# Kernel tuning notes

Hardware: AMD Instinct MI355X
Metric: run time of the kernel (lower is better)

## Reference

```python
import jax, jax.numpy as jnp
import numpy as np

B, H, W = 16, 32, 32
N = H * W
C_SEARCH, C_XCORR = 256, 64
C = C_SEARCH + C_XCORR          # phi_in_channels = gcn_in_channels
PHI_H = 64
GC_HID, GC_OUT = 128, 1
K_PTS = 48                       # keypoints per image
BN_EPS = 1e-5


def _build_coords_pair():
    # 8-neighbourhood pairs (distance^2 in {1,2}), exactly gen_8neigh_coords_pair
    idx = np.arange(N).reshape(H, W)
    ys, xs = np.meshgrid(np.arange(H), np.arange(W), indexing='ij')
    pairs8 = []
    for dy in (-1, 0, 1):
        for dx in (-1, 0, 1):
            if dy == 0 and dx == 0:
                continue
            ny, nx = ys + dy, xs + dx
            m = (ny >= 0) & (ny < H) & (nx >= 0) & (nx < W)
            pairs8.append(np.stack([idx[ys[m], xs[m]], idx[ny[m], nx[m]]], axis=1))
    pairs8 = np.concatenate(pairs8, 0)  # [7812, 2]
    # keypoint permutation pairs; keypoints on even coords -> disjoint from 8-neigh
    even = np.arange(0, H, 2)
    grid_idx = (even[:, None] * W + even[None, :]).reshape(-1)
    rng = np.random.default_rng(0)
    out = []
    for _ in range(B):
        kp = rng.choice(grid_idx, size=K_PTS, replace=False)
        a, b = np.meshgrid(kp, kp, indexing='ij')
        m = a != b
        kpairs = np.stack([a[m], b[m]], axis=1)  # K*(K-1) ordered pairs
        out.append(np.concatenate([kpairs, pairs8], 0))
    return np.stack(out, 0).astype(np.int32)  # [B, E, 2]


def setup_inputs() -> dict:
    key = jax.random.key(0)
    ks = jax.random.split(key, 10)
    u = lambda k, shape, s: jax.random.uniform(k, shape, jnp.float32, -s, s)
    inp = {
        'search_feature': jax.random.normal(ks[0], (B, C_SEARCH, H, W), jnp.float32),
        'xcorr_map': jax.random.normal(ks[1], (B, C_XCORR, H, W), jnp.float32),
        'coords_pair': jnp.asarray(_build_coords_pair()),
        # phi: Linear(C, PHI_H) + BN + ReLU, then Linear(PHI_H, 1) + Sigmoid
        'phi_w1': u(ks[2], (C, PHI_H), 1.0 / np.sqrt(C)),
        'phi_b1': u(ks[3], (PHI_H,), 1.0 / np.sqrt(C)),
        'bn_gamma': jnp.ones((PHI_H,), jnp.float32),
        'bn_beta': jnp.zeros((PHI_H,), jnp.float32),
        'phi_w2': u(ks[4], (PHI_H, 1), 1.0 / np.sqrt(PHI_H)),
        'phi_b2': u(ks[5], (1,), 1.0 / np.sqrt(PHI_H)),
        # GCN weights, torch init: uniform(-1/sqrt(out), 1/sqrt(out))
        'gc1_w': u(ks[6], (C, GC_HID), 1.0 / np.sqrt(GC_HID)),
        'gc2_w': u(ks[7], (GC_HID, GC_OUT), 1.0 / np.sqrt(GC_OUT)),
    }
    return inp


def reference(search_feature, xcorr_map, coords_pair, phi_w1, phi_b1,
              bn_gamma, bn_beta, phi_w2, phi_b2, gc1_w, gc2_w):
    # catted feature flattened: [B, C, N] (row-major h*W+w, matches torch view)
    feat = jnp.concatenate([search_feature, xcorr_map], axis=1).reshape(B, C, N)

    def per_image(f, pairs):  # f: [C, N], pairs: [E, 2]
        diff = jnp.abs(f[:, pairs[:, 0]] - f[:, pairs[:, 1]]).T  # [E, C]
        h = diff @ phi_w1 + phi_b1                                # [E, PHI_H]
        mu = jnp.mean(h, axis=0)
        var = jnp.var(h, axis=0)  # biased, as torch BN training mode
        h = (h - mu) / jnp.sqrt(var + BN_EPS) * bn_gamma + bn_beta
        h = jax.nn.relu(h)
        edge = jax.nn.sigmoid(h @ phi_w2 + phi_b2)[:, 0]          # [E]
        adj = jnp.zeros((N, N), jnp.float32).at[pairs[:, 0], pairs[:, 1]].set(edge)
        return adj

    adj = jax.vmap(per_image)(feat, coords_pair)  # [B, N, N]

    node_feat = feat.transpose(0, 2, 1)  # [B, N, C] (gcn_process_feat_xcorr=True)
    h = jax.nn.leaky_relu(jnp.einsum('bnm,bmd->bnd', adj, node_feat @ gc1_w), 0.2)
    mask = jax.nn.sigmoid(jnp.einsum('bnm,bmd->bnd', adj, h @ gc2_w))  # [B, N, 1]
    return mask[:, :, 0].reshape(B, 1, H, W)
```

## Files before the change

kernel.cpp:

```cpp
#include <hip/hip_runtime.h>
#include <hip/hip_bf16.h>

#define BB 16
#define NN 1024
#define CS 256
#define CX 64
#define CC 320
#define PH 64
#define GH 128
#define ELLW 64
#define NENG 7812
#define ROWP 324
#define RSTR 100
#define NKPH 1128

typedef __hip_bfloat16 bf16;
typedef __attribute__((ext_vector_type(8))) __bf16 bfrag;
typedef __attribute__((ext_vector_type(4))) float v4f;

__device__ __forceinline__ void tri_decode(int m, int& a, int& y) {
    float s = sqrtf((float)(9025 - 8 * m));
    int aa = (int)((95.0f - s) * 0.5f);
    if (aa > 0 && 47 * aa - (aa * (aa - 1)) / 2 > m) --aa;
    while (47 * (aa + 1) - ((aa + 1) * aa) / 2 <= m) ++aa;
    a = aa;
    y = aa + 1 + (m - (47 * aa - (aa * (aa - 1)) / 2));
}

__global__ __launch_bounds__(256) void k_prep(
    const float* __restrict__ w1, const float* __restrict__ gc1w,
    __bf16* __restrict__ whi, __bf16* __restrict__ wlo,
    __bf16* __restrict__ gwhi, __bf16* __restrict__ gwlo,
    int* __restrict__ cnt, float* __restrict__ Ssum, float* __restrict__ S2sum)
{
    int idx = blockIdx.x * 256 + threadIdx.x;
    if (idx < 10 * 4 * 64 * 8) {
        int j    = idx & 7;
        int lane = (idx >> 3) & 63;
        int nt   = (idx >> 9) & 3;
        int ks   = idx >> 11;
        int k = ks * 32 + (lane >> 4) * 8 + j;
        int n = nt * 16 + (lane & 15);
        float w = w1[k * PH + n];
        __bf16 h = (__bf16)w;
        whi[idx] = h;
        wlo[idx] = (__bf16)(w - (float)h);
    }
    if (idx < 10 * 8 * 64 * 8) {
        int j    = idx & 7;
        int lane = (idx >> 3) & 63;
        int nt   = (idx >> 9) & 7;
        int ks   = idx >> 12;
        int k = ks * 32 + (lane >> 4) * 8 + j;
        int n = nt * 16 + (lane & 15);
        float w = gc1w[k * GH + n];
        __bf16 h = (__bf16)w;
        gwhi[idx] = h;
        gwlo[idx] = (__bf16)(w - (float)h);
    }
    if (idx < BB * NN) cnt[idx] = 0;
    if (idx < BB * PH) { Ssum[idx] = 0.f; S2sum[idx] = 0.f; }
}

__global__ __launch_bounds__(256) void k_transpose(
    const float* __restrict__ search, const float* __restrict__ xcorr,
    float* __restrict__ featT)
{
    __shared__ float tile[32][33];
    int blk = blockIdx.x;
    int b   = blk % BB;
    int rem = blk / BB;
    int ct  = rem >> 5;
    int ntl = rem & 31;
    int tid = threadIdx.x;
    int cl = tid >> 5, nl = tid & 31;
    const float* sb = search + (size_t)b * CS * NN;
    const float* xb = xcorr + (size_t)b * CX * NN;
    #pragma unroll
    for (int f = 0; f < 4; ++f) {
        int c = ct * 32 + cl + f * 8;
        int n = ntl * 32 + nl;
        float v = (c < CS) ? sb[(size_t)c * NN + n] : xb[(size_t)(c - CS) * NN + n];
        tile[cl + f * 8][nl] = v;
    }
    __syncthreads();
    #pragma unroll
    for (int f = 0; f < 4; ++f) {
        int nr = cl + f * 8;
        int cc = nl;
        featT[((size_t)b * NN + ntl * 32 + nr) * CC + ct * 32 + cc] = tile[cc][nr];
    }
}

__global__ __launch_bounds__(512, 1) void k_edge(
    const float* __restrict__ featT, const int* __restrict__ pairs,
    const uint4* __restrict__ wglob, const float* __restrict__ b1,
    bf16* __restrict__ hstore, float* __restrict__ Ssum,
    float* __restrict__ S2sum, int E, int EKP, int nNG)
{
    __shared__ ushort Wsh[40960];
    __shared__ float RowsBuf[16000];
    __shared__ int kpn[48];

    int t = threadIdx.x;
    int wave = t >> 6, lane = t & 63;
    int q = lane >> 4, r = lane & 15;

    {
        uint4* dst = (uint4*)Wsh;
        #pragma unroll
        for (int k = 0; k < 10; ++k)
            dst[t + k * 512] = wglob[t + k * 512];
    }
    const bfrag* WH = (const bfrag*)Wsh;
    const bfrag* WL = (const bfrag*)(Wsh + 20480);

    float b1v[4];
    #pragma unroll
    for (int nt = 0; nt < 4; ++nt) b1v[nt] = b1[nt * 16 + r];
    float ps[4], ps2[4];
    #pragma unroll
    for (int nt = 0; nt < 4; ++nt) { ps[nt] = 0.f; ps2[nt] = 0.f; }
    int b;

    if (blockIdx.x < nNG) {
        b = blockIdx.x % BB;
        int s = blockIdx.x / BB;

        const int dyT[4] = {-1,-1,-1, 0};
        const int dxT[4] = {-1, 0, 1,-1};
        const int pfT8[8] = {0, 961, 1953, 2914, 3906, 4898, 5859, 6851};

        int d = wave >> 1;
        int p = wave & 1;
        int dy = dyT[d], dx = dxT[d];
        int y0 = dy < 0 ? 1 : 0;
        int x0 = dx < 0 ? 1 : 0;
        int x0R = dx > 0 ? 1 : 0;
        int ww = (dx == 0) ? 32 : 31;
        int pfF = pfT8[d];
        int pfR = pfT8[7 - d];
        int y = 2 * s + p;

        const float* rowI[2];
        const float* rowJ[2];
        #pragma unroll
        for (int mt = 0; mt < 2; ++mt) {
            int x  = (mt << 4) + r;
            int lr = 1 + p;
            int ni = lr * 32 + x;
            int xj = x + dx; xj = xj < 0 ? 0 : (xj > 31 ? 31 : xj);
            int nj = (lr + dy) * 32 + xj;
            rowI[mt] = &RowsBuf[ni * RSTR + q * 8];
            rowJ[mt] = &RowsBuf[nj * RSTR + q * 8];
        }

        v4f acc[2][4];
        #pragma unroll
        for (int mt = 0; mt < 2; ++mt)
            #pragma unroll
            for (int nt = 0; nt < 4; ++nt) acc[mt][nt] = (v4f)0.f;

        #pragma unroll
        for (int ph = 0; ph < 4; ++ph) {
            __syncthreads();
            const int ch0 = ph * 96;
            const int nf4 = (ph < 3) ? 24 : 8;
            for (int uu = t; uu < 96 * nf4; uu += 512) {
                int node = uu / nf4, c4 = uu - node * nf4;
                int gy = 2 * s - 1 + (node >> 5);
                if (gy >= 0) {
                    int gn = gy * 32 + (node & 31);
                    float4 v = *(const float4*)&featT[((size_t)b * NN + gn) * CC
                                                      + ch0 + c4 * 4];
                    *(float4*)&RowsBuf[node * RSTR + c4 * 4] = v;
                }
            }
            __syncthreads();

            const int ksBeg = ph * 3;
            const int ksEnd = (ph < 3) ? ksBeg + 3 : 10;
            #pragma unroll
            for (int ks = ksBeg; ks < ksEnd; ++ks) {
                int lc = ks * 32 - ch0;
                #pragma unroll
                for (int mt = 0; mt < 2; ++mt) {
                    float4 fi0 = *(const float4*)(rowI[mt] + lc);
                    float4 fi1 = *(const float4*)(rowI[mt] + lc + 4);
                    float4 fj0 = *(const float4*)(rowJ[mt] + lc);
                    float4 fj1 = *(const float4*)(rowJ[mt] + lc + 4);
                    float df[8];
                    df[0] = fabsf(fi0.x - fj0.x); df[1] = fabsf(fi0.y - fj0.y);
                    df[2] = fabsf(fi0.z - fj0.z); df[3] = fabsf(fi0.w - fj0.w);
                    df[4] = fabsf(fi1.x - fj1.x); df[5] = fabsf(fi1.y - fj1.y);
                    df[6] = fabsf(fi1.z - fj1.z); df[7] = fabsf(fi1.w - fj1.w);

                    bfrag ah, al;
                    #pragma unroll
                    for (int kk = 0; kk < 8; ++kk) {
                        __bf16 h = (__bf16)df[kk];
                        ah[kk] = h;
                        al[kk] = (__bf16)(df[kk] - (float)h);
                    }
                    #pragma unroll
                    for (int nt = 0; nt < 4; ++nt) {
                        bfrag bh = WH[((ks * 4 + nt) << 6) + lane];
                        bfrag bl = WL[((ks * 4 + nt) << 6) + lane];
                        acc[mt][nt] = __builtin_amdgcn_mfma_f32_16x16x32_bf16(
                            ah, bh, acc[mt][nt], 0, 0, 0);
                        acc[mt][nt] = __builtin_amdgcn_mfma_f32_16x16x32_bf16(
                            ah, bl, acc[mt][nt], 0, 0, 0);
                        acc[mt][nt] = __builtin_amdgcn_mfma_f32_16x16x32_bf16(
                            al, bh, acc[mt][nt], 0, 0, 0);
                    }
                }
            }
        }

        #pragma unroll
        for (int mt = 0; mt < 2; ++mt) {
            #pragma unroll
            for (int reg = 0; reg < 4; ++reg) {
                int xi = (mt << 4) + q * 4 + reg;
                int y2 = y + dy, x2 = xi + dx;
                bool valid = ((unsigned)y2 < 32u) && ((unsigned)x2 < 32u);
                if (valid) {
                    int e1 = EKP + pfF + (y - y0) * ww + (xi - x0);
                    int e2 = EKP + pfR + y2 * ww + (x2 - x0R);
                    bf16* h1 = hstore + ((size_t)b * E + e1) * PH + r;
                    bf16* h2 = hstore + ((size_t)b * E + e2) * PH + r;
                    #pragma unroll
                    for (int nt = 0; nt < 4; ++nt) {
                        float v = acc[mt][nt][reg] + b1v[nt];
                        bf16 vb = __float2bfloat16(v);
                        h1[nt * 16] = vb;
                        h2[nt * 16] = vb;
                        ps[nt] += v;
                        ps2[nt] = fmaf(v, v, ps2[nt]);
                    }
                }
            }
        }
    } else {
        int idx2 = blockIdx.x - nNG;
        b = idx2 % BB;
        int e0h = (idx2 / BB) * 128;
        if (t < 48) kpn[t] = pairs[((size_t)b * E + t * 47) * 2];
        __syncthreads();

        {
            const float4* src = (const float4*)featT;
            #pragma unroll
            for (int k = 0; k < 8; ++k) {
                int idx = t + k * 512;
                if (idx < 48 * 80) {
                    int slot = idx / 80, c4 = idx - slot * 80;
                    float4 v = src[((size_t)b * NN + kpn[slot]) * 80 + c4];
                    *(float4*)&RowsBuf[slot * ROWP + c4 * 4] = v;
                }
            }
        }

        int mA = e0h + wave * 16 + r;
        if (mA >= NKPH) mA = NKPH - 1;
        int aI, yI;
        tri_decode(mA, aI, yI);
        const float* rI = &RowsBuf[aI * ROWP + q * 8];
        const float* rJ = &RowsBuf[yI * ROWP + q * 8];

        v4f acc[4];
        #pragma unroll
        for (int nt = 0; nt < 4; ++nt) acc[nt] = (v4f)0.f;

        __syncthreads();

        #pragma unroll
        for (int ks = 0; ks < 10; ++ks) {
            float4 fi0 = *(const float4*)(rI + ks * 32);
            float4 fi1 = *(const float4*)(rI + ks * 32 + 4);
            float4 fj0 = *(const float4*)(rJ + ks * 32);
            float4 fj1 = *(const float4*)(rJ + ks * 32 + 4);
            float df[8];
            df[0] = fabsf(fi0.x - fj0.x); df[1] = fabsf(fi0.y - fj0.y);
            df[2] = fabsf(fi0.z - fj0.z); df[3] = fabsf(fi0.w - fj0.w);
            df[4] = fabsf(fi1.x - fj1.x); df[5] = fabsf(fi1.y - fj1.y);
            df[6] = fabsf(fi1.z - fj1.z); df[7] = fabsf(fi1.w - fj1.w);

            bfrag ah, al;
            #pragma unroll
            for (int kk = 0; kk < 8; ++kk) {
                __bf16 h = (__bf16)df[kk];
                ah[kk] = h;
                al[kk] = (__bf16)(df[kk] - (float)h);
            }
            #pragma unroll
            for (int nt = 0; nt < 4; ++nt) {
                bfrag bh = WH[((ks * 4 + nt) << 6) + lane];
                bfrag bl = WL[((ks * 4 + nt) << 6) + lane];
                acc[nt] = __builtin_amdgcn_mfma_f32_16x16x32_bf16(ah, bh, acc[nt], 0, 0, 0);
                acc[nt] = __builtin_amdgcn_mfma_f32_16x16x32_bf16(ah, bl, acc[nt], 0, 0, 0);
                acc[nt] = __builtin_amdgcn_mfma_f32_16x16x32_bf16(al, bh, acc[nt], 0, 0, 0);
            }
        }

        #pragma unroll
        for (int reg = 0; reg < 4; ++reg) {
            int mC = e0h + wave * 16 + q * 4 + reg;
            if (mC < NKPH) {
                int a, y;
                tri_decode(mC, a, y);
                int e1 = a * 47 + y - 1;
                int e2 = y * 47 + a;
                bf16* h1 = hstore + ((size_t)b * E + e1) * PH + r;
                bf16* h2 = hstore + ((size_t)b * E + e2) * PH + r;
                #pragma unroll
                for (int nt = 0; nt < 4; ++nt) {
                    float v = acc[nt][reg] + b1v[nt];
                    bf16 vb = __float2bfloat16(v);
                    h1[nt * 16] = vb;
                    h2[nt * 16] = vb;
                    ps[nt] += v;
                    ps2[nt] = fmaf(v, v, ps2[nt]);
                }
            }
        }
    }

    __syncthreads();
    float* sS  = RowsBuf;
    float* sS2 = RowsBuf + PH;
    if (t < PH) { sS[t] = 0.f; sS2[t] = 0.f; }
    __syncthreads();
    #pragma unroll
    for (int nt = 0; nt < 4; ++nt) {
        float p1 = ps[nt]  + __shfl_xor(ps[nt], 16, 64);
        p1 += __shfl_xor(p1, 32, 64);
        float p2 = ps2[nt] + __shfl_xor(ps2[nt], 16, 64);
        p2 += __shfl_xor(p2, 32, 64);
        if (lane < 16) {
            atomicAdd(&sS[nt * 16 + r],  2.0f * p1);
            atomicAdd(&sS2[nt * 16 + r], 2.0f * p2);
        }
    }
    __syncthreads();
    if (t < PH) {
        atomicAdd(&Ssum[b * PH + t],  sS[t]);
        atomicAdd(&S2sum[b * PH + t], sS2[t]);
    }
}

__global__ __launch_bounds__(256) void k_edge_val(
    const bf16* __restrict__ hstore, const float* __restrict__ Ssum,
    const float* __restrict__ S2sum, const float* __restrict__ gamma,
    const float* __restrict__ beta, const float* __restrict__ w2,
    const float* __restrict__ b2, const int* __restrict__ pairs,
    int* __restrict__ cnt, int* __restrict__ ecol, float* __restrict__ eval_,
    int E)
{
    __shared__ float ca[PH], cb[PH];
    int b = blockIdx.x % BB;
    int e = (blockIdx.x / BB) * 256 + threadIdx.x;
    if (threadIdx.x < PH) {
        int l = threadIdx.x;
        float mu = Ssum[b * PH + l] / E;
        float var = S2sum[b * PH + l] / E - mu * mu;
        float A = rsqrtf(var + 1e-5f) * gamma[l];
        ca[l] = A;
        cb[l] = beta[l] - mu * A;
    }
    __syncthreads();
    if (e >= E) return;
    const bfrag* hp = (const bfrag*)(hstore + ((size_t)b * E + e) * PH);
    float acc = 0.f;
    #pragma unroll
    for (int l8 = 0; l8 < 8; ++l8) {
        bfrag hv = hp[l8];
        #pragma unroll
        for (int c = 0; c < 8; ++c) {
            int l = l8 * 8 + c;
            float x = fmaf((float)hv[c], ca[l], cb[l]);
            x = x > 0.f ? x : 0.f;
            acc = fmaf(x, w2[l], acc);
        }
    }
    float edge = 1.f / (1.f + __expf(-(acc + b2[0])));
    const int* cp = pairs + ((size_t)b * E + e) * 2;
    int i = cp[0], j = cp[1];
    int row = b * NN + i;
    int slot = atomicAdd(&cnt[row], 1);
    if (slot < ELLW) {
        ecol[row * ELLW + slot]  = j;
        eval_[row * ELLW + slot] = edge;
    }
}

__global__ __launch_bounds__(256, 2) void k_gc1(
    const float* __restrict__ featT, const __bf16* __restrict__ gwhi,
    const __bf16* __restrict__ gwlo, float* __restrict__ g1)
{
    __shared__ ushort WG[40960];

    int t = threadIdx.x;
    int b = blockIdx.x % BB;
    int rem = blockIdx.x / BB;
    int half = rem & 1;
    int m0 = b * NN + (rem >> 1) * 64;

    {
        uint4* dst = (uint4*)WG;
        const uint4* sh = (const uint4*)gwhi;
        const uint4* sl = (const uint4*)gwlo;
        #pragma unroll
        for (int k = 0; k < 10; ++k) {
            int u = t + k * 256;
            int chunk = u >> 6, v = u & 63;
            int ks = chunk >> 2, ntp = chunk & 3;
            int src = (ks * 8 + half * 4 + ntp) * 64 + v;
            dst[u]        = sh[src];
            dst[2560 + u] = sl[src];
        }
    }

    int wave = t >> 6, lane = t & 63;
    int q = lane >> 4, r = lane & 15;
    const float* fp = featT + (size_t)(m0 + wave * 16 + r) * CC + q * 8;

    float fa[2][8];
    auto LOADA = [&](int ks, int buf) {
        const float4* p = (const float4*)(fp + ks * 32);
        *(float4*)&fa[buf][0] = p[0];
        *(float4*)&fa[buf][4] = p[1];
    };

    v4f acc[4];
    #pragma unroll
    for (int nt = 0; nt < 4; ++nt) acc[nt] = (v4f)0.f;

    LOADA(0, 0);
    __syncthreads();

    const bfrag* WGH = (const bfrag*)WG;
    const bfrag* WGL = (const bfrag*)(WG + 20480);

    #pragma unroll
    for (int ks = 0; ks < 10; ++ks) {
        int cur = ks & 1;
        if (ks < 9) LOADA(ks + 1, cur ^ 1);
        bfrag ah, al;
        #pragma unroll
        for (int kk = 0; kk < 8; ++kk) {
            float d = fa[cur][kk];
            __bf16 h = (__bf16)d;
            ah[kk] = h;
            al[kk] = (__bf16)(d - (float)h);
        }
        #pragma unroll
        for (int nt = 0; nt < 4; ++nt) {
            bfrag bh = WGH[((ks * 4 + nt) << 6) + lane];
            bfrag bl = WGL[((ks * 4 + nt) << 6) + lane];
            acc[nt] = __builtin_amdgcn_mfma_f32_16x16x32_bf16(ah, bh, acc[nt], 0, 0, 0);
            acc[nt] = __builtin_amdgcn_mfma_f32_16x16x32_bf16(ah, bl, acc[nt], 0, 0, 0);
            acc[nt] = __builtin_amdgcn_mfma_f32_16x16x32_bf16(al, bh, acc[nt], 0, 0, 0);
        }
    }
    #pragma unroll
    for (int nt = 0; nt < 4; ++nt) {
        #pragma unroll
        for (int reg = 0; reg < 4; ++reg) {
            int m = m0 + wave * 16 + q * 4 + reg;
            g1[(size_t)m * GH + (half * 4 + nt) * 16 + r] = acc[nt][reg];
        }
    }
}

__global__ __launch_bounds__(64) void k_spmm1(
    const float* __restrict__ g1, const int* __restrict__ cnt,
    const int* __restrict__ ecol, const float* __restrict__ eval_,
    const float* __restrict__ w2g, float* __restrict__ g2)
{
    int tid = threadIdx.x;
    int b = blockIdx.x % BB;
    int node = b * NN + blockIdx.x / BB;
    float wa = w2g[2 * tid], wb = w2g[2 * tid + 1];
    int c = cnt[node];
    const int* ec = ecol + (size_t)node * ELLW;
    const float* ev = eval_ + (size_t)node * ELLW;
    const float2* g1v = (const float2*)g1;
    float aa = 0.f, ab = 0.f;
    int s = 0;
    for (; s + 4 <= c; s += 4) {
        int j0 = ec[s], j1 = ec[s + 1], j2 = ec[s + 2], j3 = ec[s + 3];
        float v0 = ev[s], v1 = ev[s + 1], v2 = ev[s + 2], v3 = ev[s + 3];
        float2 u0 = g1v[((size_t)b * NN + j0) * 64 + tid];
        float2 u1 = g1v[((size_t)b * NN + j1) * 64 + tid];
        float2 u2 = g1v[((size_t)b * NN + j2) * 64 + tid];
        float2 u3 = g1v[((size_t)b * NN + j3) * 64 + tid];
        aa = fmaf(v0, u0.x, aa); ab = fmaf(v0, u0.y, ab);
        aa = fmaf(v1, u1.x, aa); ab = fmaf(v1, u1.y, ab);
        aa = fmaf(v2, u2.x, aa); ab = fmaf(v2, u2.y, ab);
        aa = fmaf(v3, u3.x, aa); ab = fmaf(v3, u3.y, ab);
    }
    for (; s < c; ++s) {
        float2 u = g1v[((size_t)b * NN + ec[s]) * 64 + tid];
        float v = ev[s];
        aa = fmaf(v, u.x, aa); ab = fmaf(v, u.y, ab);
    }
    float h1a = aa > 0.f ? aa : 0.2f * aa;
    float h1b = ab > 0.f ? ab : 0.2f * ab;
    float p = h1a * wa + h1b * wb;
    #pragma unroll
    for (int off = 32; off >= 1; off >>= 1) p += __shfl_down(p, off, 64);
    if (tid == 0) g2[node] = p;
}

__global__ __launch_bounds__(64) void k_spmm2(
    const float* __restrict__ g2, const int* __restrict__ cnt,
    const int* __restrict__ ecol, const float* __restrict__ eval_,
    float* __restrict__ out)
{
    int b = blockIdx.x % BB;
    int node = b * NN + blockIdx.x / BB;
    int lane = threadIdx.x;
    int c = cnt[node];
    float p = 0.f;
    if (lane < c) {
        int j = ecol[(size_t)node * ELLW + lane];
        p = eval_[(size_t)node * ELLW + lane] * g2[b * NN + j];
    }
    #pragma unroll
    for (int off = 32; off >= 1; off >>= 1) p += __shfl_down(p, off, 64);
    if (lane == 0) out[node] = 1.f / (1.f + __expf(-p));
}

extern "C" void kernel_launch(void* const* d_in, const int* in_sizes, int n_in,
                              void* d_out, int out_size, void* d_ws, size_t ws_size,
                              hipStream_t stream)
{
    const float* search = (const float*)d_in[0];
    const float* xcorr  = (const float*)d_in[1];
    const int*   pairs  = (const int*)d_in[2];
    const float* w1     = (const float*)d_in[3];
    const float* b1     = (const float*)d_in[4];
    const float* gamma  = (const float*)d_in[5];
    const float* beta   = (const float*)d_in[6];
    const float* w2     = (const float*)d_in[7];
    const float* b2     = (const float*)d_in[8];
    const float* gc1w   = (const float*)d_in[9];
    const float* gc2w   = (const float*)d_in[10];
    float* out = (float*)d_out;

    int E   = in_sizes[2] / (BB * 2);
    int EKP = E - NENG;
    int nb   = (E + 255) / 256;
    int nbKP = (NKPH + 127) / 128;
    int nNG  = BB * 16;

    char* ws = (char*)d_ws;
    size_t off = 0;
    auto alloc = [&](size_t bytes) {
        size_t o = off;
        off += (bytes + 255) & ~(size_t)255;
        return o;
    };
    __bf16* whi   = (__bf16*)(ws + alloc(10 * 4 * 64 * 8 * 2));
    __bf16* wlo   = (__bf16*)(ws + alloc(10 * 4 * 64 * 8 * 2));
    __bf16* gwhi  = (__bf16*)(ws + alloc(10 * 8 * 64 * 8 * 2));
    __bf16* gwlo  = (__bf16*)(ws + alloc(10 * 8 * 64 * 8 * 2));
    float* featT  = (float*)(ws + alloc((size_t)BB * NN * CC * 4));
    bf16*  hstore = (bf16*)(ws + alloc((size_t)BB * E * PH * 2));
    float* Ssum   = (float*)(ws + alloc(BB * PH * 4));
    float* S2sum  = (float*)(ws + alloc(BB * PH * 4));
    int*   cnt    = (int*)(ws + alloc(BB * NN * 4));
    int*   ecol   = (int*)(ws + alloc((size_t)BB * NN * ELLW * 4));
    float* eval_  = (float*)(ws + alloc((size_t)BB * NN * ELLW * 4));
    float* g1     = (float*)(ws + alloc((size_t)BB * NN * GH * 4));
    float* g2     = (float*)(ws + alloc(BB * NN * 4));
    (void)ws_size; (void)n_in; (void)out_size;

    k_prep<<<dim3(160), dim3(256), 0, stream>>>(w1, gc1w, whi, wlo, gwhi, gwlo,
                                                cnt, Ssum, S2sum);
    k_transpose<<<dim3(BB * 320), dim3(256), 0, stream>>>(search, xcorr, featT);
    k_edge<<<dim3(nNG + BB * nbKP), dim3(512), 0, stream>>>(featT, pairs,
                                                            (const uint4*)whi, b1,
                                                            hstore, Ssum, S2sum,
                                                            E, EKP, nNG);
    k_edge_val<<<dim3(BB * nb), dim3(256), 0, stream>>>(hstore, Ssum, S2sum,
                                                        gamma, beta, w2, b2,
                                                        pairs, cnt, ecol, eval_, E);
    k_gc1<<<dim3(BB * 32), dim3(256), 0, stream>>>(featT, gwhi, gwlo, g1);
    k_spmm1<<<dim3(BB * NN), dim3(64), 0, stream>>>(g1, cnt, ecol, eval_, gc2w, g2);
    k_spmm2<<<dim3(BB * NN), dim3(64), 0, stream>>>(g2, cnt, ecol, eval_, out);
}
```

Before: 161.1 us.

## Merge independent kernels into shared launches and pack four nodes per SpMM block

Merges the weight-prep and transpose kernels into one launch by dispatching on block index. It does the same for the edge-value/ELL-build kernel and the gc1 GEMM, which are independent, so they can run concurrently and two launch gaps disappear. Both SpMM kernels now process four nodes per 256-thread block instead of one node per 64-thread block, which cuts the block count by four. The mixed launches may see some imbalance, and the edge-value blocks now reserve the GEMM's large shared allocation, which may reduce their occupancy.

```diff
diff --git a/kernel.cpp b/kernel.cpp
--- a/kernel.cpp
+++ b/kernel.cpp
@@ -27,68 +27,67 @@
     y = aa + 1 + (m - (47 * aa - (aa * (aa - 1)) / 2));
 }
 
-__global__ __launch_bounds__(256) void k_prep(
+__global__ __launch_bounds__(256) void k_prep_transpose(
+    const float* __restrict__ search, const float* __restrict__ xcorr,
+    float* __restrict__ featT,
     const float* __restrict__ w1, const float* __restrict__ gc1w,
     __bf16* __restrict__ whi, __bf16* __restrict__ wlo,
     __bf16* __restrict__ gwhi, __bf16* __restrict__ gwlo,
     int* __restrict__ cnt, float* __restrict__ Ssum, float* __restrict__ S2sum)
 {
-    int idx = blockIdx.x * 256 + threadIdx.x;
-    if (idx < 10 * 4 * 64 * 8) {
-        int j    = idx & 7;
-        int lane = (idx >> 3) & 63;
-        int nt   = (idx >> 9) & 3;
-        int ks   = idx >> 11;
-        int k = ks * 32 + (lane >> 4) * 8 + j;
-        int n = nt * 16 + (lane & 15);
-        float w = w1[k * PH + n];
-        __bf16 h = (__bf16)w;
-        whi[idx] = h;
-        wlo[idx] = (__bf16)(w - (float)h);
-    }
-    if (idx < 10 * 8 * 64 * 8) {
-        int j    = idx & 7;
-        int lane = (idx >> 3) & 63;
-        int nt   = (idx >> 9) & 7;
-        int ks   = idx >> 12;
-        int k = ks * 32 + (lane >> 4) * 8 + j;
-        int n = nt * 16 + (lane & 15);
-        float w = gc1w[k * GH + n];
-        __bf16 h = (__bf16)w;
-        gwhi[idx] = h;
-        gwlo[idx] = (__bf16)(w - (float)h);
-    }
-    if (idx < BB * NN) cnt[idx] = 0;
-    if (idx < BB * PH) { Ssum[idx] = 0.f; S2sum[idx] = 0.f; }
-}
-
-__global__ __launch_bounds__(256) void k_transpose(
-    const float* __restrict__ search, const float* __restrict__ xcorr,
-    float* __restrict__ featT)
-{
     __shared__ float tile[32][33];
     int blk = blockIdx.x;
-    int b   = blk % BB;
-    int rem = blk / BB;
-    int ct  = rem >> 5;
-    int ntl = rem & 31;
     int tid = threadIdx.x;
-    int cl = tid >> 5, nl = tid & 31;
-    const float* sb = search + (size_t)b * CS * NN;
-    const float* xb = xcorr + (size_t)b * CX * NN;
-    #pragma unroll
-    for (int f = 0; f < 4; ++f) {
-        int c = ct * 32 + cl + f * 8;
-        int n = ntl * 32 + nl;
-        float v = (c < CS) ? sb[(size_t)c * NN + n] : xb[(size_t)(c - CS) * NN + n];
-        tile[cl + f * 8][nl] = v;
-    }
-    __syncthreads();
-    #pragma unroll
-    for (int f = 0; f < 4; ++f) {
-        int nr = cl + f * 8;
-        int cc = nl;
-        featT[((size_t)b * NN + ntl * 32 + nr) * CC + ct * 32 + cc] = tile[cc][nr];
+    if (blk < BB * 320) {
+        int b   = blk % BB;
+        int rem = blk / BB;
+        int ct  = rem >> 5;
+        int ntl = rem & 31;
+        int cl = tid >> 5, nl = tid & 31;
+        const float* sb = search + (size_t)b * CS * NN;
+        const float* xb = xcorr + (size_t)b * CX * NN;
+        #pragma unroll
+        for (int f = 0; f < 4; ++f) {
+            int c = ct * 32 + cl + f * 8;
+            int n = ntl * 32 + nl;
+            float v = (c < CS) ? sb[(size_t)c * NN + n] : xb[(size_t)(c - CS) * NN + n];
+            tile[cl + f * 8][nl] = v;
+        }
+        __syncthreads();
+        #pragma unroll
+        for (int f = 0; f < 4; ++f) {
+            int nr = cl + f * 8;
+            int cc = nl;
+            featT[((size_t)b * NN + ntl * 32 + nr) * CC + ct * 32 + cc] = tile[cc][nr];
+        }
+    } else {
+        int idx = (blk - BB * 320) * 256 + tid;
+        if (idx < 10 * 4 * 64 * 8) {
+            int j    = idx & 7;
+            int lane = (idx >> 3) & 63;
+            int nt   = (idx >> 9) & 3;
+            int ks   = idx >> 11;
+            int k = ks * 32 + (lane >> 4) * 8 + j;
+            int n = nt * 16 + (lane & 15);
+            float w = w1[k * PH + n];
+            __bf16 h = (__bf16)w;
+            whi[idx] = h;
+            wlo[idx] = (__bf16)(w - (float)h);
+        }
+        if (idx < 10 * 8 * 64 * 8) {
+            int j    = idx & 7;
+            int lane = (idx >> 3) & 63;
+            int nt   = (idx >> 9) & 7;
+            int ks   = idx >> 12;
+            int k = ks * 32 + (lane >> 4) * 8 + j;
+            int n = nt * 16 + (lane & 15);
+            float w = gc1w[k * GH + n];
+            __bf16 h = (__bf16)w;
+            gwhi[idx] = h;
+            gwlo[idx] = (__bf16)(w - (float)h);
+        }
+        if (idx < BB * NN) cnt[idx] = 0;
+        if (idx < BB * PH) { Ssum[idx] = 0.f; S2sum[idx] = 0.f; }
     }
 }
 
@@ -349,138 +348,139 @@
     }
 }
 
-__global__ __launch_bounds__(256) void k_edge_val(
+__global__ __launch_bounds__(256, 2) void k_val_gc1(
+    const float* __restrict__ featT, const __bf16* __restrict__ gwhi,
+    const __bf16* __restrict__ gwlo, float* __restrict__ g1,
     const bf16* __restrict__ hstore, const float* __restrict__ Ssum,
     const float* __restrict__ S2sum, const float* __restrict__ gamma,
     const float* __restrict__ beta, const float* __restrict__ w2,
     const float* __restrict__ b2, const int* __restrict__ pairs,
     int* __restrict__ cnt, int* __restrict__ ecol, float* __restrict__ eval_,
-    int E)
-{
-    __shared__ float ca[PH], cb[PH];
-    int b = blockIdx.x % BB;
-    int e = (blockIdx.x / BB) * 256 + threadIdx.x;
-    if (threadIdx.x < PH) {
-        int l = threadIdx.x;
-        float mu = Ssum[b * PH + l] / E;
-        float var = S2sum[b * PH + l] / E - mu * mu;
-        float A = rsqrtf(var + 1e-5f) * gamma[l];
-        ca[l] = A;
-        cb[l] = beta[l] - mu * A;
-    }
-    __syncthreads();
-    if (e >= E) return;
-    const bfrag* hp = (const bfrag*)(hstore + ((size_t)b * E + e) * PH);
-    float acc = 0.f;
-    #pragma unroll
-    for (int l8 = 0; l8 < 8; ++l8) {
-        bfrag hv = hp[l8];
-        #pragma unroll
-        for (int c = 0; c < 8; ++c) {
-            int l = l8 * 8 + c;
-            float x = fmaf((float)hv[c], ca[l], cb[l]);
-            x = x > 0.f ? x : 0.f;
-            acc = fmaf(x, w2[l], acc);
-        }
-    }
-    float edge = 1.f / (1.f + __expf(-(acc + b2[0])));
-    const int* cp = pairs + ((size_t)b * E + e) * 2;
-    int i = cp[0], j = cp[1];
-    int row = b * NN + i;
-    int slot = atomicAdd(&cnt[row], 1);
-    if (slot < ELLW) {
-        ecol[row * ELLW + slot]  = j;
-        eval_[row * ELLW + slot] = edge;
-    }
-}
-
-__global__ __launch_bounds__(256, 2) void k_gc1(
-    const float* __restrict__ featT, const __bf16* __restrict__ gwhi,
-    const __bf16* __restrict__ gwlo, float* __restrict__ g1)
+    int E, int nGC)
 {
     __shared__ ushort WG[40960];
 
     int t = threadIdx.x;
-    int b = blockIdx.x % BB;
-    int rem = blockIdx.x / BB;
-    int half = rem & 1;
-    int m0 = b * NN + (rem >> 1) * 64;
-
-    {
-        uint4* dst = (uint4*)WG;
-        const uint4* sh = (const uint4*)gwhi;
-        const uint4* sl = (const uint4*)gwlo;
-        #pragma unroll
-        for (int k = 0; k < 10; ++k) {
-            int u = t + k * 256;
-            int chunk = u >> 6, v = u & 63;
-            int ks = chunk >> 2, ntp = chunk & 3;
-            int src = (ks * 8 + half * 4 + ntp) * 64 + v;
-            dst[u]        = sh[src];
-            dst[2560 + u] = sl[src];
-        }
-    }
-
-    int wave = t >> 6, lane = t & 63;
-    int q = lane >> 4, r = lane & 15;
-    const float* fp = featT + (size_t)(m0 + wave * 16 + r) * CC + q * 8;
-
-    float fa[2][8];
-    auto LOADA = [&](int ks, int buf) {
-        const float4* p = (const float4*)(fp + ks * 32);
-        *(float4*)&fa[buf][0] = p[0];
-        *(float4*)&fa[buf][4] = p[1];
-    };
-
-    v4f acc[4];
-    #pragma unroll
-    for (int nt = 0; nt < 4; ++nt) acc[nt] = (v4f)0.f;
-
-    LOADA(0, 0);
-    __syncthreads();
-
-    const bfrag* WGH = (const bfrag*)WG;
-    const bfrag* WGL = (const bfrag*)(WG + 20480);
-
-    #pragma unroll
-    for (int ks = 0; ks < 10; ++ks) {
-        int cur = ks & 1;
-        if (ks < 9) LOADA(ks + 1, cur ^ 1);
-        bfrag ah, al;
-        #pragma unroll
-        for (int kk = 0; kk < 8; ++kk) {
-            float d = fa[cur][kk];
-            __bf16 h = (__bf16)d;
-            ah[kk] = h;
-            al[kk] = (__bf16)(d - (float)h);
+    if ((int)blockIdx.x < nGC) {
+        int b = blockIdx.x % BB;
+        int rem = blockIdx.x / BB;
+        int half = rem & 1;
+        int m0 = b * NN + (rem >> 1) * 64;
+
+        {
+            uint4* dst = (uint4*)WG;
+            const uint4* sh = (const uint4*)gwhi;
+            const uint4* sl = (const uint4*)gwlo;
+            #pragma unroll
+            for (int k = 0; k < 10; ++k) {
+                int u = t + k * 256;
+                int chunk = u >> 6, v = u & 63;
+                int ks = chunk >> 2, ntp = chunk & 3;
+                int src = (ks * 8 + half * 4 + ntp) * 64 + v;
+                dst[u]        = sh[src];
+                dst[2560 + u] = sl[src];
+            }
+        }
+
+        int wave = t >> 6, lane = t & 63;
+        int q = lane >> 4, r = lane & 15;
+        const float* fp = featT + (size_t)(m0 + wave * 16 + r) * CC + q * 8;
+
+        float fa[2][8];
+        auto LOADA = [&](int ks, int buf) {
+            const float4* p = (const float4*)(fp + ks * 32);
+            *(float4*)&fa[buf][0] = p[0];
+            *(float4*)&fa[buf][4] = p[1];
+        };
+
+        v4f acc[4];
+        #pragma unroll
+        for (int nt = 0; nt < 4; ++nt) acc[nt] = (v4f)0.f;
+
+        LOADA(0, 0);
+        __syncthreads();
+
+        const bfrag* WGH = (const bfrag*)WG;
+        const bfrag* WGL = (const bfrag*)(WG + 20480);
+
+        #pragma unroll
+        for (int ks = 0; ks < 10; ++ks) {
+            int cur = ks & 1;
+            if (ks < 9) LOADA(ks + 1, cur ^ 1);
+            bfrag ah, al;
+            #pragma unroll
+            for (int kk = 0; kk < 8; ++kk) {
+                float d = fa[cur][kk];
+                __bf16 h = (__bf16)d;
+                ah[kk] = h;
+                al[kk] = (__bf16)(d - (float)h);
+            }
+            #pragma unroll
+            for (int nt = 0; nt < 4; ++nt) {
+                bfrag bh = WGH[((ks * 4 + nt) << 6) + lane];
+                bfrag bl = WGL[((ks * 4 + nt) << 6) + lane];
+                acc[nt] = __builtin_amdgcn_mfma_f32_16x16x32_bf16(ah, bh, acc[nt], 0, 0, 0);
+                acc[nt] = __builtin_amdgcn_mfma_f32_16x16x32_bf16(ah, bl, acc[nt], 0, 0, 0);
+                acc[nt] = __builtin_amdgcn_mfma_f32_16x16x32_bf16(al, bh, acc[nt], 0, 0, 0);
+            }
         }
         #pragma unroll
         for (int nt = 0; nt < 4; ++nt) {
-            bfrag bh = WGH[((ks * 4 + nt) << 6) + lane];
-            bfrag bl = WGL[((ks * 4 + nt) << 6) + lane];
-            acc[nt] = __builtin_amdgcn_mfma_f32_16x16x32_bf16(ah, bh, acc[nt], 0, 0, 0);
-            acc[nt] = __builtin_amdgcn_mfma_f32_16x16x32_bf16(ah, bl, acc[nt], 0, 0, 0);
-            acc[nt] = __builtin_amdgcn_mfma_f32_16x16x32_bf16(al, bh, acc[nt], 0, 0, 0);
-        }
-    }
-    #pragma unroll
-    for (int nt = 0; nt < 4; ++nt) {
-        #pragma unroll
-        for (int reg = 0; reg < 4; ++reg) {
-            int m = m0 + wave * 16 + q * 4 + reg;
-            g1[(size_t)m * GH + (half * 4 + nt) * 16 + r] = acc[nt][reg];
-        }
-    }
-}
-
-__global__ __launch_bounds__(64) void k_spmm1(
+            #pragma unroll
+            for (int reg = 0; reg < 4; ++reg) {
+                int m = m0 + wave * 16 + q * 4 + reg;
+                g1[(size_t)m * GH + (half * 4 + nt) * 16 + r] = acc[nt][reg];
+            }
+        }
+    } else {
+        float* ca = (float*)WG;
+        float* cb = ca + PH;
+        int blk = blockIdx.x - nGC;
+        int b = blk % BB;
+        int e = (blk / BB) * 256 + t;
+        if (t < PH) {
+            int l = t;
+            float mu = Ssum[b * PH + l] / E;
+            float var = S2sum[b * PH + l] / E - mu * mu;
+            float A = rsqrtf(var + 1e-5f) * gamma[l];
+            ca[l] = A;
+            cb[l] = beta[l] - mu * A;
+        }
+        __syncthreads();
+        if (e >= E) return;
+        const bfrag* hp = (const bfrag*)(hstore + ((size_t)b * E + e) * PH);
+        float acc = 0.f;
+        #pragma unroll
+        for (int l8 = 0; l8 < 8; ++l8) {
+            bfrag hv = hp[l8];
+            #pragma unroll
+            for (int c = 0; c < 8; ++c) {
+                int l = l8 * 8 + c;
+                float x = fmaf((float)hv[c], ca[l], cb[l]);
+                x = x > 0.f ? x : 0.f;
+                acc = fmaf(x, w2[l], acc);
+            }
+        }
+        float edge = 1.f / (1.f + __expf(-(acc + b2[0])));
+        const int* cp = pairs + ((size_t)b * E + e) * 2;
+        int i = cp[0], j = cp[1];
+        int row = b * NN + i;
+        int slot = atomicAdd(&cnt[row], 1);
+        if (slot < ELLW) {
+            ecol[row * ELLW + slot]  = j;
+            eval_[row * ELLW + slot] = edge;
+        }
+    }
+}
+
+__global__ __launch_bounds__(256) void k_spmm1(
     const float* __restrict__ g1, const int* __restrict__ cnt,
     const int* __restrict__ ecol, const float* __restrict__ eval_,
     const float* __restrict__ w2g, float* __restrict__ g2)
 {
-    int tid = threadIdx.x;
-    int b = blockIdx.x % BB;
-    int node = b * NN + blockIdx.x / BB;
+    int tid = threadIdx.x & 63;
+    int node = blockIdx.x * 4 + (threadIdx.x >> 6);
+    int base = node & ~(NN - 1);
     float wa = w2g[2 * tid], wb = w2g[2 * tid + 1];
     int c = cnt[node];
     const int* ec = ecol + (size_t)node * ELLW;
@@ -491,17 +491,17 @@
     for (; s + 4 <= c; s += 4) {
         int j0 = ec[s], j1 = ec[s + 1], j2 = ec[s + 2], j3 = ec[s + 3];
         float v0 = ev[s], v1 = ev[s + 1], v2 = ev[s + 2], v3 = ev[s + 3];
-        float2 u0 = g1v[((size_t)b * NN + j0) * 64 + tid];
-        float2 u1 = g1v[((size_t)b * NN + j1) * 64 + tid];
-        float2 u2 = g1v[((size_t)b * NN + j2) * 64 + tid];
-        float2 u3 = g1v[((size_t)b * NN + j3) * 64 + tid];
+        float2 u0 = g1v[((size_t)(base + j0)) * 64 + tid];
+        float2 u1 = g1v[((size_t)(base + j1)) * 64 + tid];
+        float2 u2 = g1v[((size_t)(base + j2)) * 64 + tid];
+        float2 u3 = g1v[((size_t)(base + j3)) * 64 + tid];
         aa = fmaf(v0, u0.x, aa); ab = fmaf(v0, u0.y, ab);
         aa = fmaf(v1, u1.x, aa); ab = fmaf(v1, u1.y, ab);
         aa = fmaf(v2, u2.x, aa); ab = fmaf(v2, u2.y, ab);
         aa = fmaf(v3, u3.x, aa); ab = fmaf(v3, u3.y, ab);
     }
     for (; s < c; ++s) {
-        float2 u = g1v[((size_t)b * NN + ec[s]) * 64 + tid];
+        float2 u = g1v[((size_t)(base + ec[s])) * 64 + tid];
         float v = ev[s];
         aa = fmaf(v, u.x, aa); ab = fmaf(v, u.y, ab);
     }
@@ -513,19 +513,19 @@
     if (tid == 0) g2[node] = p;
 }
 
-__global__ __launch_bounds__(64) void k_spmm2(
+__global__ __launch_bounds__(256) void k_spmm2(
     const float* __restrict__ g2, const int* __restrict__ cnt,
     const int* __restrict__ ecol, const float* __restrict__ eval_,
     float* __restrict__ out)
 {
-    int b = blockIdx.x % BB;
-    int node = b * NN + blockIdx.x / BB;
-    int lane = threadIdx.x;
+    int lane = threadIdx.x & 63;
+    int node = blockIdx.x * 4 + (threadIdx.x >> 6);
+    int base = node & ~(NN - 1);
     int c = cnt[node];
     float p = 0.f;
     if (lane < c) {
         int j = ecol[(size_t)node * ELLW + lane];
-        p = eval_[(size_t)node * ELLW + lane] * g2[b * NN + j];
+        p = eval_[(size_t)node * ELLW + lane] * g2[base + j];
     }
     #pragma unroll
     for (int off = 32; off >= 1; off >>= 1) p += __shfl_down(p, off, 64);
@@ -554,6 +554,7 @@
     int nb   = (E + 255) / 256;
     int nbKP = (NKPH + 127) / 128;
     int nNG  = BB * 16;
+    int nGC  = BB * 32;
 
     char* ws = (char*)d_ws;
     size_t off = 0;
@@ -577,17 +578,16 @@
     float* g2     = (float*)(ws + alloc(BB * NN * 4));
     (void)ws_size; (void)n_in; (void)out_size;
 
-    k_prep<<<dim3(160), dim3(256), 0, stream>>>(w1, gc1w, whi, wlo, gwhi, gwlo,
-                                                cnt, Ssum, S2sum);
-    k_transpose<<<dim3(BB * 320), dim3(256), 0, stream>>>(search, xcorr, featT);
+    k_prep_transpose<<<dim3(BB * 320 + 160), dim3(256), 0, stream>>>(
+        search, xcorr, featT, w1, gc1w, whi, wlo, gwhi, gwlo, cnt, Ssum, S2sum);
     k_edge<<<dim3(nNG + BB * nbKP), dim3(512), 0, stream>>>(featT, pairs,
                                                             (const uint4*)whi, b1,
                                                             hstore, Ssum, S2sum,
                                                             E, EKP, nNG);
-    k_edge_val<<<dim3(BB * nb), dim3(256), 0, stream>>>(hstore, Ssum, S2sum,
-                                                        gamma, beta, w2, b2,
-                                                        pairs, cnt, ecol, eval_, E);
-    k_gc1<<<dim3(BB * 32), dim3(256), 0, stream>>>(featT, gwhi, gwlo, g1);
-    k_spmm1<<<dim3(BB * NN), dim3(64), 0, stream>>>(g1, cnt, ecol, eval_, gc2w, g2);
-    k_spmm2<<<dim3(BB * NN), dim3(64), 0, stream>>>(g2, cnt, ecol, eval_, out);
-}
+    k_val_gc1<<<dim3(nGC + BB * nb), dim3(256), 0, stream>>>(
+        featT, gwhi, gwlo, g1, hstore, Ssum, S2sum, gamma, beta, w2, b2,
+        pairs, cnt, ecol, eval_, E, nGC);
+    k_spmm1<<<dim3(BB * NN / 4), dim3(256), 0, stream>>>(g1, cnt, ecol, eval_,
+                                                         gc2w, g2);
+    k_spmm2<<<dim3(BB * NN / 4), dim3(256), 0, stream>>>(g2, cnt, ecol, eval_, out);
+}
```

New measurement: 156.8 us. 2.7% less time.
